# Performance work log

Measured on AMD Instinct MI355X. Metric: run time of the kernel, lower is better.

## Reference

```python
import jax, jax.numpy as jnp
import numpy as np

NEG_INF = -1.0e9


def setup_inputs() -> dict:
    key = jax.random.key(0)
    k1, k2, k3, k4 = jax.random.split(key, 4)
    B, N, F, U, H = 4, 2048, 128, 64, 4
    x = jax.random.normal(k1, (B, N, F), dtype=jnp.float32)
    adj = jax.random.randint(k2, (B, N, N), 0, 2, dtype=jnp.int32)
    W = jax.random.normal(k3, (H, F, U), dtype=jnp.float32) * (1.0 / np.sqrt(F))
    b = jnp.zeros((H, U), dtype=jnp.float32)
    a_w = jax.random.normal(k4, (H, U), dtype=jnp.float32) * (1.0 / np.sqrt(U))
    a_b = jnp.zeros((H,), dtype=jnp.float32)
    return {"x": x, "adj": adj, "W": W, "b": b, "a_w": a_w, "a_b": a_b}


def reference(x, adj, W, b, a_w, a_b):
    # Per-head Dense + relu, batched over heads: proj [H,B,N,U]
    proj = jax.nn.relu(jnp.einsum('bnf,hfu->hbnu', x, W) + b[:, None, None, :])
    # Scalar attention score per node: s [H,B,N]
    s = jnp.einsum('hbnu,hu->hbn', proj, a_w) + a_b[:, None, None]
    # Outer-product logits [H,B,N,N], masked by adjacency
    logits = s[:, :, :, None] * s[:, :, None, :]
    logits = jnp.where(adj[None] > 0, logits, NEG_INF)
    scores = jax.nn.softmax(logits, axis=-1)
    # Weighted aggregation, then mean over heads -> [B,N,U]
    out = jnp.einsum('hbij,hbju->hbiu', scores, proj)
    return jnp.mean(out, axis=0)
```

## Files before the change

kernel.cpp:

```cpp
#include <hip/hip_runtime.h>
#include <hip/hip_bf16.h>


#define Bdim 4
#define Ndim 2048
#define Fdim 128
#define Udim 64
#define Hdim 4
#define JC 2
#define JCHUNK (Ndim / JC)

typedef __attribute__((ext_vector_type(8))) short short8;
typedef __attribute__((ext_vector_type(4))) float f32x4;

__device__ __forceinline__ short bf16_rne(float f) {
  union { __hip_bfloat16 b; unsigned short u; } c;
  c.b = __float2bfloat16(f);
  return (short)c.u;
}

__device__ __forceinline__ void splitbf(float f, short& hi, short& lo) {
  unsigned u = __float_as_uint(f);
  hi = (short)(u >> 16);
  float lof = f - __uint_as_float(u & 0xffff0000u);
  lo = bf16_rne(lof);
}

__device__ __forceinline__ void splitpk(float w0, float w1, unsigned& hiw,
                                        unsigned& low) {
  union { __hip_bfloat162 b; unsigned u; } h, l;
  float2 wp; wp.x = w0; wp.y = w1;
  h.b = __float22bfloat162_rn(wp);
  float2 lp;
  lp.x = w0 - __bfloat162float(h.b.x);
  lp.y = w1 - __bfloat162float(h.b.y);
  l.b = __float22bfloat162_rn(lp);
  hiw = h.u;
  low = l.u;
}

__device__ __forceinline__ void stage16(const void* g, void* l) {
  __builtin_amdgcn_global_load_lds(
      (const __attribute__((address_space(1))) unsigned int*)g,
      (__attribute__((address_space(3))) unsigned int*)l, 16, 0, 0);
}

__global__ __launch_bounds__(256) void pack_adj_kernel(
    const int* __restrict__ adj, unsigned long long* __restrict__ bits,
    int nchunks) {
  const int lane = threadIdx.x & 63;
  const int wid = (blockIdx.x * 256 + threadIdx.x) >> 6;
  const int nw = (gridDim.x * 256) >> 6;
  for (int c = wid * 4; c + 3 < nchunks; c += nw * 4) {
    int v0 = adj[(size_t)(c + 0) * 64 + lane];
    int v1 = adj[(size_t)(c + 1) * 64 + lane];
    int v2 = adj[(size_t)(c + 2) * 64 + lane];
    int v3 = adj[(size_t)(c + 3) * 64 + lane];
    unsigned long long m0 = __ballot(v0 != 0);
    unsigned long long m1 = __ballot(v1 != 0);
    unsigned long long m2 = __ballot(v2 != 0);
    unsigned long long m3 = __ballot(v3 != 0);
    if (lane == 0) {
      bits[c + 0] = m0;
      bits[c + 1] = m1;
      bits[c + 2] = m2;
      bits[c + 3] = m3;
    }
  }
}

__global__ __launch_bounds__(256) void proj_kernel(
    const float* __restrict__ x, const float* __restrict__ W,
    const float* __restrict__ bias, const float* __restrict__ a_w,
    const float* __restrict__ a_b, unsigned short* __restrict__ pTh,
    unsigned short* __restrict__ pTl, float* __restrict__ s) {
  const int bid = blockIdx.x;
  const int nt = bid & 31;
  const int b = (bid >> 5) & 3;
  const int h = bid >> 7;
  const int n0 = nt * 64;

  __shared__ __align__(16) char smem[71168];
  float (*Wl)[Udim] = (float(*)[Udim])(smem);
  float (*xl)[Fdim + 4] = (float(*)[Fdim + 4])(smem + 32768);
  float (*pt)[68] = (float(*)[68])(smem + 32768);
  float* bl = (float*)(smem + 66560);
  float* awl = (float*)(smem + 66816);
  float (*sred)[16] = (float(*)[16])(smem + 67072);

  const int t = threadIdx.x;

  const float* Wg = W + (size_t)h * Fdim * Udim;
  for (int k = t; k < Fdim * Udim / 4; k += 256) {
    ((float4*)&Wl[0][0])[k] = ((const float4*)Wg)[k];
  }
  if (t < Udim) {
    bl[t] = bias[h * Udim + t];
    awl[t] = a_w[h * Udim + t];
  }
  const float* xg = x + ((size_t)b * Ndim + n0) * Fdim;
  for (int k = t; k < 64 * Fdim / 4; k += 256) {
    int row = k >> 5;
    int c4 = k & 31;
    float4 v = ((const float4*)xg)[(size_t)row * (Fdim / 4) + c4];
    *(float4*)&xl[row][c4 * 4] = v;
  }
  __syncthreads();

  const int ug = t & 15, rg = t >> 4;
  const int u0 = ug * 4, r0 = rg * 4;
  float acc[4][4] = {};

#pragma unroll 4
  for (int f = 0; f < Fdim; ++f) {
    const float4 wv = *(const float4*)&Wl[f][u0];
    const float xv[4] = {xl[r0][f], xl[r0 + 1][f], xl[r0 + 2][f], xl[r0 + 3][f]};
#pragma unroll
    for (int c = 0; c < 4; ++c) {
      acc[c][0] = fmaf(xv[c], wv.x, acc[c][0]);
      acc[c][1] = fmaf(xv[c], wv.y, acc[c][1]);
      acc[c][2] = fmaf(xv[c], wv.z, acc[c][2]);
      acc[c][3] = fmaf(xv[c], wv.w, acc[c][3]);
    }
  }

  float po[4][4];
#pragma unroll
  for (int c = 0; c < 4; ++c)
#pragma unroll
    for (int k = 0; k < 4; ++k)
      po[c][k] = fmaxf(acc[c][k] + bl[u0 + k], 0.f);

#pragma unroll
  for (int c = 0; c < 4; ++c) {
    float sp = po[c][0] * awl[u0 + 0] + po[c][1] * awl[u0 + 1] +
               po[c][2] * awl[u0 + 2] + po[c][3] * awl[u0 + 3];
    sred[r0 + c][ug] = sp;
  }
  __syncthreads();

#pragma unroll
  for (int k = 0; k < 4; ++k) {
    float4 v = {po[0][k], po[1][k], po[2][k], po[3][k]};
    *(float4*)&pt[u0 + k][r0] = v;
  }
  __syncthreads();

  const size_t hb = (size_t)h * Bdim + b;
  const int su = t >> 2;
  const int snl = (t & 3) * 16;
  float v[16];
#pragma unroll
  for (int j = 0; j < 4; ++j)
    *(float4*)&v[4 * j] = *(const float4*)&pt[su][snl + 4 * j];
  short hi[16], lo[16];
#pragma unroll
  for (int k = 0; k < 16; ++k) splitbf(v[k], hi[k], lo[k]);
  unsigned short* ph =
      pTh + hb * (size_t)(Udim * Ndim) + (size_t)su * Ndim + n0 + snl;
  unsigned short* pl =
      pTl + hb * (size_t)(Udim * Ndim) + (size_t)su * Ndim + n0 + snl;
  *(short8*)(ph + 0) = *(short8*)&hi[0];
  *(short8*)(ph + 8) = *(short8*)&hi[8];
  *(short8*)(pl + 0) = *(short8*)&lo[0];
  *(short8*)(pl + 8) = *(short8*)&lo[8];

  if (t < 64) {
    float sum = a_b[h];
#pragma unroll
    for (int k = 0; k < 16; ++k) sum += sred[t][k];
    s[hb * Ndim + n0 + t] = sum;
  }
}

#define ASTEP(BPTR, JS)                                                        \
  do {                                                                         \
    const unsigned int mb = (ab[irow][(JS) >> 5] >> (q * 8)) & 0xffu;          \
    const f32x4 s0 = *(const f32x4*)&sj[(JS) + q * 8];                         \
    const f32x4 s1 = *(const f32x4*)&sj[(JS) + q * 8 + 4];                     \
    const float sv[8] = {s0.x, s0.y, s0.z, s0.w, s1.x, s1.y, s1.z, s1.w};      \
    float w[8];                                                                \
    _Pragma("unroll") for (int e = 0; e < 8; ++e) {                            \
      float we = __builtin_amdgcn_exp2f(si2 * sv[e]);                          \
      w[e] = ((mb >> e) & 1u) ? we : 0.f;                                      \
    }                                                                          \
    union { short8 s8; unsigned u[4]; } ahi, alo;                              \
    _Pragma("unroll") for (int p = 0; p < 4; ++p)                              \
      splitpk(w[2 * p], w[2 * p + 1], ahi.u[p], alo.u[p]);                     \
    const short* bp = (const short*)(BPTR);                                    \
    const short8 b0h = *(const short8*)(bp + 0 * 512 + lane * 8);              \
    const short8 b0l = *(const short8*)(bp + 1 * 512 + lane * 8);              \
    const short8 b1h = *(const short8*)(bp + 2 * 512 + lane * 8);              \
    const short8 b1l = *(const short8*)(bp + 3 * 512 + lane * 8);              \
    const short8 b2h = *(const short8*)(bp + 4 * 512 + lane * 8);              \
    const short8 b2l = *(const short8*)(bp + 5 * 512 + lane * 8);              \
    const short8 b3h = *(const short8*)(bp + 6 * 512 + lane * 8);              \
    const short8 b3l = *(const short8*)(bp + 7 * 512 + lane * 8);              \
    __builtin_amdgcn_s_setprio(1);                                             \
    acc[0] = __builtin_amdgcn_mfma_f32_16x16x32_bf16(ahi.s8, b0h, acc[0],0,0,0);\
    acc[1] = __builtin_amdgcn_mfma_f32_16x16x32_bf16(ahi.s8, b1h, acc[1],0,0,0);\
    acc[2] = __builtin_amdgcn_mfma_f32_16x16x32_bf16(ahi.s8, b2h, acc[2],0,0,0);\
    acc[3] = __builtin_amdgcn_mfma_f32_16x16x32_bf16(ahi.s8, b3h, acc[3],0,0,0);\
    accZ   = __builtin_amdgcn_mfma_f32_16x16x32_bf16(ahi.s8, bones, accZ,0,0,0);\
    acc[0] = __builtin_amdgcn_mfma_f32_16x16x32_bf16(alo.s8, b0h, acc[0],0,0,0);\
    acc[1] = __builtin_amdgcn_mfma_f32_16x16x32_bf16(alo.s8, b1h, acc[1],0,0,0);\
    acc[2] = __builtin_amdgcn_mfma_f32_16x16x32_bf16(alo.s8, b2h, acc[2],0,0,0);\
    acc[3] = __builtin_amdgcn_mfma_f32_16x16x32_bf16(alo.s8, b3h, acc[3],0,0,0);\
    accZ   = __builtin_amdgcn_mfma_f32_16x16x32_bf16(alo.s8, bones, accZ,0,0,0);\
    acc[0] = __builtin_amdgcn_mfma_f32_16x16x32_bf16(ahi.s8, b0l, acc[0],0,0,0);\
    acc[1] = __builtin_amdgcn_mfma_f32_16x16x32_bf16(ahi.s8, b1l, acc[1],0,0,0);\
    acc[2] = __builtin_amdgcn_mfma_f32_16x16x32_bf16(ahi.s8, b2l, acc[2],0,0,0);\
    acc[3] = __builtin_amdgcn_mfma_f32_16x16x32_bf16(ahi.s8, b3l, acc[3],0,0,0);\
    __builtin_amdgcn_s_setprio(0);                                             \
  } while (0)

__global__ __launch_bounds__(256, 4) void attn_mfma_kernel(
    const unsigned short* __restrict__ pTh,
    const unsigned short* __restrict__ pTl, const float* __restrict__ s,
    const unsigned int* __restrict__ abits, float* __restrict__ out_part,
    float* __restrict__ Z_part) {
  const int bid = blockIdx.x;
  const int jc = bid & 1;
  const int it = (bid >> 1) & 31;
  const int b = (bid >> 6) & 3;
  const int h = bid >> 8;
  const int i0g = it * 64;
  const int j0g = jc * JCHUNK;

  __shared__ float sj[JCHUNK];
  __shared__ unsigned int ab[64][33];
  __shared__ __align__(16) short Bst[3][8][512];

  const int t = threadIdx.x;
  const int wv = t >> 6;
  const int lane = t & 63;
  const int q = lane >> 4;
  const int li = lane & 15;
  const size_t hb = (size_t)h * Bdim + b;
  const float* sg = s + hb * Ndim;

  ((float4*)sj)[t] = ((const float4*)(sg + j0g))[t];
  for (int k = t; k < 64 * 32; k += 256) {
    int row = k >> 5, w = k & 31;
    ab[row][w] =
        abits[((size_t)b * Ndim + i0g + row) * (Ndim / 32) + (j0g >> 5) + w];
  }
  const int irow = wv * 16 + li;
  const float si2 = sg[i0g + irow] * 1.4426950408889634f;

  const unsigned short* bsrc_h =
      pTh + hb * (size_t)(Udim * Ndim) + (size_t)(wv * 16 + li) * Ndim + j0g +
      q * 8;
  const unsigned short* bsrc_l =
      pTl + hb * (size_t)(Udim * Ndim) + (size_t)(wv * 16 + li) * Ndim + j0g +
      q * 8;

  __syncthreads();

  stage16(bsrc_h + 0, &Bst[0][wv * 2 + 0][0]);
  stage16(bsrc_l + 0, &Bst[0][wv * 2 + 1][0]);
  stage16(bsrc_h + 32, &Bst[1][wv * 2 + 0][0]);
  stage16(bsrc_l + 32, &Bst[1][wv * 2 + 1][0]);

  f32x4 acc[4] = {};
  f32x4 accZ = {};
  const short8 bones = {16256, 16256, 16256, 16256,
                        16256, 16256, 16256, 16256};

  short* bS0 = &Bst[0][0][0];
  short* bS1 = &Bst[1][0][0];
  short* bS2 = &Bst[2][0][0];

  for (int js = 0; js < JCHUNK; js += 32) {
    asm volatile("s_waitcnt vmcnt(2)" ::: "memory");
    __builtin_amdgcn_s_barrier();
    __builtin_amdgcn_sched_barrier(0);
    const int jsn = (js + 64) & (JCHUNK - 1);
    stage16(bsrc_h + jsn, bS2 + (wv * 2 + 0) * 512);
    stage16(bsrc_l + jsn, bS2 + (wv * 2 + 1) * 512);
    ASTEP(bS0, js);
    short* tmp = bS0; bS0 = bS1; bS1 = bS2; bS2 = tmp;
  }

  const size_t pslab = ((size_t)h * JC + jc) * Bdim + b;
  if (li == 0) {
#pragma unroll
    for (int r = 0; r < 4; ++r)
      Z_part[pslab * Ndim + i0g + wv * 16 + q * 4 + r] = accZ[r];
  }

  float* op = out_part + (pslab * Ndim + i0g + wv * 16) * Udim;
#pragma unroll
  for (int r = 0; r < 4; ++r) {
    const int ir = q * 4 + r;
#pragma unroll
    for (int m = 0; m < 4; ++m) {
      op[(size_t)ir * Udim + m * 16 + li] = acc[m][r];
    }
  }
}

__global__ __launch_bounds__(256) void combine_kernel(
    const float* __restrict__ out_part, const float* __restrict__ Z_part,
    float* __restrict__ out) {
  const int idx = blockIdx.x * 256 + threadIdx.x;
  const int u4 = idx & 15;
  const size_t bn = (size_t)(idx >> 4);
  float4 r = {0.f, 0.f, 0.f, 0.f};
#pragma unroll
  for (int h = 0; h < Hdim; ++h) {
    float4 p = {0.f, 0.f, 0.f, 0.f};
    float z = 0.f;
#pragma unroll
    for (int j = 0; j < JC; ++j) {
      const size_t sl = ((size_t)h * JC + j) * (Bdim * Ndim) + bn;
      float4 pj = ((const float4*)out_part)[sl * (Udim / 4) + u4];
      p.x += pj.x; p.y += pj.y; p.z += pj.z; p.w += pj.w;
      z += Z_part[sl];
    }
    z = (z != 0.f) ? z : 1.f;
    const float inv = 1.f / z;
    r.x += p.x * inv;
    r.y += p.y * inv;
    r.z += p.z * inv;
    r.w += p.w * inv;
  }
  r.x *= 0.25f; r.y *= 0.25f; r.z *= 0.25f; r.w *= 0.25f;
  ((float4*)out)[idx] = r;
}

extern "C" void kernel_launch(void* const* d_in, const int* in_sizes, int n_in,
                              void* d_out, int out_size, void* d_ws,
                              size_t ws_size, hipStream_t stream) {
  const float* x = (const float*)d_in[0];
  const int* adj = (const int*)d_in[1];
  const float* W = (const float*)d_in[2];
  const float* bias = (const float*)d_in[3];
  const float* a_w = (const float*)d_in[4];
  const float* a_b = (const float*)d_in[5];
  float* out = (float*)d_out;

  char* ws = (char*)d_ws;
  unsigned short* pTh = (unsigned short*)(ws + 0);
  unsigned short* pTl = (unsigned short*)(ws + 4194304);
  float* s = (float*)(ws + 8388608);
  unsigned int* adjbits = (unsigned int*)(ws + 8519680);
  float* out_part = (float*)(ws + 10616832);
  float* Z_part = (float*)(ws + 27394048);

  const int nchunks = Bdim * Ndim * Ndim / 64;
  pack_adj_kernel<<<2048, 256, 0, stream>>>(adj, (unsigned long long*)adjbits,
                                            nchunks);
  proj_kernel<<<Hdim * Bdim * 32, 256, 0, stream>>>(x, W, bias, a_w, a_b, pTh,
                                                    pTl, s);
  attn_mfma_kernel<<<Hdim * Bdim * 32 * JC, 256, 0, stream>>>(
      pTh, pTl, s, adjbits, out_part, Z_part);
  combine_kernel<<<(Bdim * Ndim * Udim / 4) / 256, 256, 0, stream>>>(
      out_part, Z_part, out);
}
```

Baseline: 162.9 us.

## Replace split-bf16 triple MFMA with single fp16 MFMA using max-shifted exponent

The attention kernel previously split weights and projected values into bf16 hi/lo pairs and ran three MFMA passes to emulate fp32. It now stores projections as fp16 and runs one fp16 MFMA pass per step. To keep exp values within fp16 range, each block computes the max |s| for its (h,b) and subtracts |s_i|*M inside the exponent. This cuts MFMA work by about 3x and halves the B-operand staging traffic, at the cost of fp16 precision and an extra reduction pass over s. Block indices are also remapped so related blocks land on the same XCD.

```diff
diff --git a/kernel.cpp b/kernel.cpp
--- a/kernel.cpp
+++ b/kernel.cpp
@@ -1,5 +1,6 @@
 #include <hip/hip_runtime.h>
 #include <hip/hip_bf16.h>
+#include <hip/hip_fp16.h>
 
 
 #define Bdim 4
@@ -11,33 +12,8 @@
 #define JCHUNK (Ndim / JC)
 
 typedef __attribute__((ext_vector_type(8))) short short8;
+typedef __attribute__((ext_vector_type(8))) _Float16 half8;
 typedef __attribute__((ext_vector_type(4))) float f32x4;
-
-__device__ __forceinline__ short bf16_rne(float f) {
-  union { __hip_bfloat16 b; unsigned short u; } c;
-  c.b = __float2bfloat16(f);
-  return (short)c.u;
-}
-
-__device__ __forceinline__ void splitbf(float f, short& hi, short& lo) {
-  unsigned u = __float_as_uint(f);
-  hi = (short)(u >> 16);
-  float lof = f - __uint_as_float(u & 0xffff0000u);
-  lo = bf16_rne(lof);
-}
-
-__device__ __forceinline__ void splitpk(float w0, float w1, unsigned& hiw,
-                                        unsigned& low) {
-  union { __hip_bfloat162 b; unsigned u; } h, l;
-  float2 wp; wp.x = w0; wp.y = w1;
-  h.b = __float22bfloat162_rn(wp);
-  float2 lp;
-  lp.x = w0 - __bfloat162float(h.b.x);
-  lp.y = w1 - __bfloat162float(h.b.y);
-  l.b = __float22bfloat162_rn(lp);
-  hiw = h.u;
-  low = l.u;
-}
 
 __device__ __forceinline__ void stage16(const void* g, void* l) {
   __builtin_amdgcn_global_load_lds(
@@ -72,8 +48,8 @@
 __global__ __launch_bounds__(256) void proj_kernel(
     const float* __restrict__ x, const float* __restrict__ W,
     const float* __restrict__ bias, const float* __restrict__ a_w,
-    const float* __restrict__ a_b, unsigned short* __restrict__ pTh,
-    unsigned short* __restrict__ pTl, float* __restrict__ s) {
+    const float* __restrict__ a_b, unsigned short* __restrict__ pT,
+    float* __restrict__ s) {
   const int bid = blockIdx.x;
   const int nt = bid & 31;
   const int b = (bid >> 5) & 3;
@@ -153,17 +129,22 @@
 #pragma unroll
   for (int j = 0; j < 4; ++j)
     *(float4*)&v[4 * j] = *(const float4*)&pt[su][snl + 4 * j];
-  short hi[16], lo[16];
-#pragma unroll
-  for (int k = 0; k < 16; ++k) splitbf(v[k], hi[k], lo[k]);
+  unsigned ow[8];
+#pragma unroll
+  for (int p2 = 0; p2 < 8; ++p2) {
+    float2 fp;
+    fp.x = v[2 * p2];
+    fp.y = v[2 * p2 + 1];
+    union { __half2 h; unsigned u; } cc;
+    cc.h = __float22half2_rn(fp);
+    ow[p2] = cc.u;
+  }
   unsigned short* ph =
-      pTh + hb * (size_t)(Udim * Ndim) + (size_t)su * Ndim + n0 + snl;
-  unsigned short* pl =
-      pTl + hb * (size_t)(Udim * Ndim) + (size_t)su * Ndim + n0 + snl;
-  *(short8*)(ph + 0) = *(short8*)&hi[0];
-  *(short8*)(ph + 8) = *(short8*)&hi[8];
-  *(short8*)(pl + 0) = *(short8*)&lo[0];
-  *(short8*)(pl + 8) = *(short8*)&lo[8];
+      pT + hb * (size_t)(Udim * Ndim) + (size_t)su * Ndim + n0 + snl;
+  uint4 w0v; w0v.x = ow[0]; w0v.y = ow[1]; w0v.z = ow[2]; w0v.w = ow[3];
+  uint4 w1v; w1v.x = ow[4]; w1v.y = ow[5]; w1v.z = ow[6]; w1v.w = ow[7];
+  *(uint4*)(ph) = w0v;
+  *(uint4*)(ph + 8) = w1v;
 
   if (t < 64) {
     float sum = a_b[h];
@@ -176,60 +157,57 @@
 #define ASTEP(BPTR, JS)                                                        \
   do {                                                                         \
     const unsigned int mb = (ab[irow][(JS) >> 5] >> (q * 8)) & 0xffu;          \
-    const f32x4 s0 = *(const f32x4*)&sj[(JS) + q * 8];                         \
-    const f32x4 s1 = *(const f32x4*)&sj[(JS) + q * 8 + 4];                     \
-    const float sv[8] = {s0.x, s0.y, s0.z, s0.w, s1.x, s1.y, s1.z, s1.w};      \
+    const f32x4 s0v = *(const f32x4*)&sj[(JS) + q * 8];                        \
+    const f32x4 s1v = *(const f32x4*)&sj[(JS) + q * 8 + 4];                    \
+    const float sv[8] = {s0v.x, s0v.y, s0v.z, s0v.w,                           \
+                         s1v.x, s1v.y, s1v.z, s1v.w};                          \
     float w[8];                                                                \
     _Pragma("unroll") for (int e = 0; e < 8; ++e) {                            \
-      float we = __builtin_amdgcn_exp2f(si2 * sv[e]);                          \
+      float we = __builtin_amdgcn_exp2f(fmaf(si2, sv[e], nc));                 \
       w[e] = ((mb >> e) & 1u) ? we : 0.f;                                      \
     }                                                                          \
-    union { short8 s8; unsigned u[4]; } ahi, alo;                              \
-    _Pragma("unroll") for (int p = 0; p < 4; ++p)                              \
-      splitpk(w[2 * p], w[2 * p + 1], ahi.u[p], alo.u[p]);                     \
+    union { half8 h; unsigned u[4]; } af;                                      \
+    _Pragma("unroll") for (int p2 = 0; p2 < 4; ++p2) {                         \
+      float2 fp;                                                               \
+      fp.x = w[2 * p2];                                                        \
+      fp.y = w[2 * p2 + 1];                                                    \
+      union { __half2 h; unsigned u; } cc;                                     \
+      cc.h = __float22half2_rn(fp);                                            \
+      af.u[p2] = cc.u;                                                         \
+    }                                                                          \
     const short* bp = (const short*)(BPTR);                                    \
-    const short8 b0h = *(const short8*)(bp + 0 * 512 + lane * 8);              \
-    const short8 b0l = *(const short8*)(bp + 1 * 512 + lane * 8);              \
-    const short8 b1h = *(const short8*)(bp + 2 * 512 + lane * 8);              \
-    const short8 b1l = *(const short8*)(bp + 3 * 512 + lane * 8);              \
-    const short8 b2h = *(const short8*)(bp + 4 * 512 + lane * 8);              \
-    const short8 b2l = *(const short8*)(bp + 5 * 512 + lane * 8);              \
-    const short8 b3h = *(const short8*)(bp + 6 * 512 + lane * 8);              \
-    const short8 b3l = *(const short8*)(bp + 7 * 512 + lane * 8);              \
+    union { short8 s; half8 h; } b0, b1, b2, b3;                               \
+    b0.s = *(const short8*)(bp + 0 * 512 + lane * 8);                          \
+    b1.s = *(const short8*)(bp + 1 * 512 + lane * 8);                          \
+    b2.s = *(const short8*)(bp + 2 * 512 + lane * 8);                          \
+    b3.s = *(const short8*)(bp + 3 * 512 + lane * 8);                          \
     __builtin_amdgcn_s_setprio(1);                                             \
-    acc[0] = __builtin_amdgcn_mfma_f32_16x16x32_bf16(ahi.s8, b0h, acc[0],0,0,0);\
-    acc[1] = __builtin_amdgcn_mfma_f32_16x16x32_bf16(ahi.s8, b1h, acc[1],0,0,0);\
-    acc[2] = __builtin_amdgcn_mfma_f32_16x16x32_bf16(ahi.s8, b2h, acc[2],0,0,0);\
-    acc[3] = __builtin_amdgcn_mfma_f32_16x16x32_bf16(ahi.s8, b3h, acc[3],0,0,0);\
-    accZ   = __builtin_amdgcn_mfma_f32_16x16x32_bf16(ahi.s8, bones, accZ,0,0,0);\
-    acc[0] = __builtin_amdgcn_mfma_f32_16x16x32_bf16(alo.s8, b0h, acc[0],0,0,0);\
-    acc[1] = __builtin_amdgcn_mfma_f32_16x16x32_bf16(alo.s8, b1h, acc[1],0,0,0);\
-    acc[2] = __builtin_amdgcn_mfma_f32_16x16x32_bf16(alo.s8, b2h, acc[2],0,0,0);\
-    acc[3] = __builtin_amdgcn_mfma_f32_16x16x32_bf16(alo.s8, b3h, acc[3],0,0,0);\
-    accZ   = __builtin_amdgcn_mfma_f32_16x16x32_bf16(alo.s8, bones, accZ,0,0,0);\
-    acc[0] = __builtin_amdgcn_mfma_f32_16x16x32_bf16(ahi.s8, b0l, acc[0],0,0,0);\
-    acc[1] = __builtin_amdgcn_mfma_f32_16x16x32_bf16(ahi.s8, b1l, acc[1],0,0,0);\
-    acc[2] = __builtin_amdgcn_mfma_f32_16x16x32_bf16(ahi.s8, b2l, acc[2],0,0,0);\
-    acc[3] = __builtin_amdgcn_mfma_f32_16x16x32_bf16(ahi.s8, b3l, acc[3],0,0,0);\
+    acc[0] = __builtin_amdgcn_mfma_f32_16x16x32_f16(af.h, b0.h, acc[0],0,0,0); \
+    acc[1] = __builtin_amdgcn_mfma_f32_16x16x32_f16(af.h, b1.h, acc[1],0,0,0); \
+    acc[2] = __builtin_amdgcn_mfma_f32_16x16x32_f16(af.h, b2.h, acc[2],0,0,0); \
+    acc[3] = __builtin_amdgcn_mfma_f32_16x16x32_f16(af.h, b3.h, acc[3],0,0,0); \
+    accZ = __builtin_amdgcn_mfma_f32_16x16x32_f16(af.h, ones.h, accZ,0,0,0);   \
     __builtin_amdgcn_s_setprio(0);                                             \
   } while (0)
 
 __global__ __launch_bounds__(256, 4) void attn_mfma_kernel(
-    const unsigned short* __restrict__ pTh,
-    const unsigned short* __restrict__ pTl, const float* __restrict__ s,
+    const unsigned short* __restrict__ pT, const float* __restrict__ s,
     const unsigned int* __restrict__ abits, float* __restrict__ out_part,
     float* __restrict__ Z_part) {
   const int bid = blockIdx.x;
-  const int jc = bid & 1;
-  const int it = (bid >> 1) & 31;
-  const int b = (bid >> 6) & 3;
-  const int h = bid >> 8;
+  const int xcd = bid & 7, slot = bid >> 3;
+  const int g = xcd + ((slot >> 5) << 3);
+  const int it = slot & 31;
+  const int jc = g & 1;
+  const int b = (g >> 1) & 3;
+  const int h = g >> 3;
   const int i0g = it * 64;
   const int j0g = jc * JCHUNK;
 
   __shared__ float sj[JCHUNK];
   __shared__ unsigned int ab[64][33];
-  __shared__ __align__(16) short Bst[3][8][512];
+  __shared__ __align__(16) short Bst[3][4][512];
+  __shared__ float mred[4];
 
   const int t = threadIdx.x;
   const int wv = t >> 6;
@@ -239,6 +217,16 @@
   const size_t hb = (size_t)h * Bdim + b;
   const float* sg = s + hb * Ndim;
 
+  float4 a0 = ((const float4*)sg)[t];
+  float4 a1 = ((const float4*)sg)[t + 256];
+  float mloc = fmaxf(
+      fmaxf(fmaxf(fabsf(a0.x), fabsf(a0.y)), fmaxf(fabsf(a0.z), fabsf(a0.w))),
+      fmaxf(fmaxf(fabsf(a1.x), fabsf(a1.y)), fmaxf(fabsf(a1.z), fabsf(a1.w))));
+#pragma unroll
+  for (int off = 1; off < 64; off <<= 1)
+    mloc = fmaxf(mloc, __shfl_xor(mloc, off, 64));
+  if (lane == 0) mred[wv] = mloc;
+
   ((float4*)sj)[t] = ((const float4*)(sg + j0g))[t];
   for (int k = t; k < 64 * 32; k += 256) {
     int row = k >> 5, w = k & 31;
@@ -247,37 +235,33 @@
   }
   const int irow = wv * 16 + li;
   const float si2 = sg[i0g + irow] * 1.4426950408889634f;
-
-  const unsigned short* bsrc_h =
-      pTh + hb * (size_t)(Udim * Ndim) + (size_t)(wv * 16 + li) * Ndim + j0g +
+  __syncthreads();
+  const float M = fmaxf(fmaxf(mred[0], mred[1]), fmaxf(mred[2], mred[3]));
+  const float nc = -fabsf(si2) * M;
+
+  const unsigned short* bsrc =
+      pT + hb * (size_t)(Udim * Ndim) + (size_t)(wv * 16 + li) * Ndim + j0g +
       q * 8;
-  const unsigned short* bsrc_l =
-      pTl + hb * (size_t)(Udim * Ndim) + (size_t)(wv * 16 + li) * Ndim + j0g +
-      q * 8;
-
-  __syncthreads();
-
-  stage16(bsrc_h + 0, &Bst[0][wv * 2 + 0][0]);
-  stage16(bsrc_l + 0, &Bst[0][wv * 2 + 1][0]);
-  stage16(bsrc_h + 32, &Bst[1][wv * 2 + 0][0]);
-  stage16(bsrc_l + 32, &Bst[1][wv * 2 + 1][0]);
+
+  stage16(bsrc + 0, &Bst[0][wv][0]);
+  stage16(bsrc + 32, &Bst[1][wv][0]);
 
   f32x4 acc[4] = {};
   f32x4 accZ = {};
-  const short8 bones = {16256, 16256, 16256, 16256,
-                        16256, 16256, 16256, 16256};
+  union { half8 h; short8 s8; } ones;
+#pragma unroll
+  for (int e = 0; e < 8; ++e) ones.h[e] = (_Float16)1.0f;
 
   short* bS0 = &Bst[0][0][0];
   short* bS1 = &Bst[1][0][0];
   short* bS2 = &Bst[2][0][0];
 
   for (int js = 0; js < JCHUNK; js += 32) {
-    asm volatile("s_waitcnt vmcnt(2)" ::: "memory");
+    asm volatile("s_waitcnt vmcnt(1)" ::: "memory");
     __builtin_amdgcn_s_barrier();
     __builtin_amdgcn_sched_barrier(0);
     const int jsn = (js + 64) & (JCHUNK - 1);
-    stage16(bsrc_h + jsn, bS2 + (wv * 2 + 0) * 512);
-    stage16(bsrc_l + jsn, bS2 + (wv * 2 + 1) * 512);
+    stage16(bsrc + jsn, bS2 + wv * 512);
     ASTEP(bS0, js);
     short* tmp = bS0; bS0 = bS1; bS1 = bS2; bS2 = tmp;
   }
@@ -341,20 +325,19 @@
   float* out = (float*)d_out;
 
   char* ws = (char*)d_ws;
-  unsigned short* pTh = (unsigned short*)(ws + 0);
-  unsigned short* pTl = (unsigned short*)(ws + 4194304);
-  float* s = (float*)(ws + 8388608);
-  unsigned int* adjbits = (unsigned int*)(ws + 8519680);
-  float* out_part = (float*)(ws + 10616832);
-  float* Z_part = (float*)(ws + 27394048);
+  unsigned short* pT = (unsigned short*)(ws + 0);
+  float* s = (float*)(ws + 4194304);
+  unsigned int* adjbits = (unsigned int*)(ws + 4325376);
+  float* out_part = (float*)(ws + 6422528);
+  float* Z_part = (float*)(ws + 23199744);
 
   const int nchunks = Bdim * Ndim * Ndim / 64;
   pack_adj_kernel<<<2048, 256, 0, stream>>>(adj, (unsigned long long*)adjbits,
                                             nchunks);
-  proj_kernel<<<Hdim * Bdim * 32, 256, 0, stream>>>(x, W, bias, a_w, a_b, pTh,
-                                                    pTl, s);
+  proj_kernel<<<Hdim * Bdim * 32, 256, 0, stream>>>(x, W, bias, a_w, a_b, pT,
+                                                    s);
   attn_mfma_kernel<<<Hdim * Bdim * 32 * JC, 256, 0, stream>>>(
-      pTh, pTl, s, adjbits, out_part, Z_part);
+      pT, s, adjbits, out_part, Z_part);
   combine_kernel<<<(Bdim * Ndim * Udim / 4) / 256, 256, 0, stream>>>(
       out_part, Z_part, out);
 }
```

After: 148.1 us. -9.1%, faster.
